# Kernel optimization log

Measured on AMD Instinct MI355X. Metric: run time of the kernel, lower is better.

## Reference

```python
import jax, jax.numpy as jnp
import numpy as np

N_NODES = 100000
N_EDGES = 3200000
IN_DIM = 4
BIG = 32
HID = 2
BN_EPS = 1e-5


def _lin_init(key, fan_in, fan_out):
    k1, k2 = jax.random.split(key)
    bound = 1.0 / np.sqrt(fan_in)
    W = jax.random.uniform(k1, (fan_in, fan_out), minval=-bound, maxval=bound, dtype=jnp.float32)
    b = jax.random.uniform(k2, (fan_out,), minval=-bound, maxval=bound, dtype=jnp.float32)
    return W, b


def setup_inputs() -> dict:
    key = jax.random.key(0)
    ks = jax.random.split(key, 12)
    x = jax.random.normal(ks[0], (N_NODES, IN_DIM), dtype=jnp.float32)
    edge_index = jax.random.randint(ks[1], (2, N_EDGES), 0, N_NODES, dtype=jnp.int32)
    eps_noise = jax.random.normal(ks[2], (N_NODES, HID), dtype=jnp.float32)
    # batchnorm affine params
    bn_gamma = jnp.ones((IN_DIM,), jnp.float32)
    bn_beta = jnp.zeros((IN_DIM,), jnp.float32)
    # encoder EdgeConv MLP: 2*IN_DIM -> BIG -> BIG
    eW1, eb1 = _lin_init(ks[3], 2 * IN_DIM, BIG)
    eW2, eb2 = _lin_init(ks[4], BIG, BIG)
    # mu / logvar heads
    mW, mb = _lin_init(ks[5], BIG, HID)
    vW, vb = _lin_init(ks[6], BIG, HID)
    # decoder EdgeConv MLP: 2*HID -> BIG -> BIG -> IN_DIM
    dW1, db1 = _lin_init(ks[7], 2 * HID, BIG)
    dW2, db2 = _lin_init(ks[8], BIG, BIG)
    dW3, db3 = _lin_init(ks[9], BIG, IN_DIM)
    return dict(x=x, edge_index=edge_index, eps_noise=eps_noise,
                bn_gamma=bn_gamma, bn_beta=bn_beta,
                eW1=eW1, eb1=eb1, eW2=eW2, eb2=eb2,
                mW=mW, mb=mb, vW=vW, vb=vb,
                dW1=dW1, db1=db1, dW2=dW2, db2=db2, dW3=dW3, db3=db3)


def _segment_mean(msgs, tgt, n):
    s = jax.ops.segment_sum(msgs, tgt, num_segments=n)
    c = jax.ops.segment_sum(jnp.ones((msgs.shape[0],), msgs.dtype), tgt, num_segments=n)
    return s / jnp.maximum(c, 1.0)[:, None]


def _edge_conv(x, edge_index, mlp):
    # PyG EdgeConv: h_i = mean_{j->i} nn([x_i, x_j - x_i])
    src, tgt = edge_index[0], edge_index[1]
    x_i = x[tgt]                      # [E, F]
    x_j = x[src]                      # [E, F]
    feat = jnp.concatenate([x_i, x_j - x_i], axis=-1)  # [E, 2F]
    msg = mlp(feat)                   # [E, F_out]
    return _segment_mean(msg, tgt, x.shape[0])


def reference(x, edge_index, eps_noise, bn_gamma, bn_beta,
              eW1, eb1, eW2, eb2, mW, mb, vW, vb,
              dW1, db1, dW2, db2, dW3, db3):
    # BatchNorm1d (training mode: batch statistics, biased variance)
    mean = jnp.mean(x, axis=0)
    var = jnp.var(x, axis=0)
    xn = (x - mean) * jax.lax.rsqrt(var + BN_EPS) * bn_gamma + bn_beta

    enc_mlp = lambda f: jax.nn.relu(jax.nn.relu(f @ eW1 + eb1) @ eW2 + eb2)
    h = _edge_conv(xn, edge_index, enc_mlp)           # [N, BIG]

    mu = h @ mW + mb                                  # [N, HID]
    log_var = h @ vW + vb                             # [N, HID]
    z = mu + eps_noise * jnp.exp(0.5 * log_var)       # reparameterize

    dec_mlp = lambda f: jax.nn.relu(jax.nn.relu(f @ dW1 + db1) @ dW2 + db2) @ dW3 + db3
    out = _edge_conv(z, edge_index, dec_mlp)          # [N, IN_DIM]
    return out, mu, log_var
```

## Files before the change

kernel.cpp:

```cpp
#include <hip/hip_runtime.h>
#include <math.h>

#define N_NODES 100000
#define N_EDGES 3200000
#define NBLK_EDGE ((N_EDGES + 255) / 256)
#define NBLK_NODE ((N_NODES + 255) / 256)

#define NB 64
#define NBUCK ((N_NODES + NB - 1) / NB)
#define NSLICE 256
#define SLICE (N_EDGES / NSLICE)
#define P2 2048

typedef _Float16 h2f16 __attribute__((ext_vector_type(2)));
typedef __fp16 f16x8 __attribute__((ext_vector_type(8)));
typedef float f32x4 __attribute__((ext_vector_type(4)));
typedef unsigned u32x4 __attribute__((ext_vector_type(4)));

#define PK_ENC_A2 0
#define PK_DEC_A2 512
#define PK_ENC_W1 1024
#define PK_DEC_W1 1152
#define PK_ENC_H 1216
#define PK_DEC_H 1280
#define PK_TOTAL 1344

__device__ __forceinline__ h2f16 mkh2(float a, float b) {
  h2f16 h;
  h.x = (_Float16)a;
  h.y = (_Float16)b;
  return h;
}
__device__ __forceinline__ float fdot2(h2f16 a, h2f16 b, float c) {
  return __builtin_amdgcn_fdot2(a, b, c, false);
}
__device__ __forceinline__ h2f16 pk(float a, float b) {
  auto r = __builtin_amdgcn_cvt_pkrtz(a, b);
  return __builtin_bit_cast(h2f16, r);
}
__device__ __forceinline__ unsigned h2u(h2f16 h) {
  return __builtin_bit_cast(unsigned, h);
}
__device__ __forceinline__ f32x4 mfma16(f16x8 a, f16x8 b, f32x4 c) {
  return __builtin_amdgcn_mfma_f32_16x16x32_f16(a, b, c, 0, 0, 0);
}

__global__ __launch_bounds__(256) void pack_weights(
    const float* __restrict__ eW1, const float* __restrict__ eW2,
    const float* __restrict__ mW, const float* __restrict__ vW,
    const float* __restrict__ dW1, const float* __restrict__ dW2,
    const float* __restrict__ dW3, h2f16* __restrict__ wpk) {
  int t = threadIdx.x;
  for (int i = t; i < 512; i += 256) {
    int tl = i >> 8, rest = i & 255, lane = rest >> 2, p = rest & 3;
    int q = lane >> 4, c = lane & 15;
    int k0 = q * 8 + 2 * p, out = 16 * tl + c;
    wpk[PK_ENC_A2 + i] = mkh2(eW2[k0 * 32 + out], eW2[(k0 + 1) * 32 + out]);
    wpk[PK_DEC_A2 + i] = mkh2(dW2[k0 * 32 + out], dW2[(k0 + 1) * 32 + out]);
  }
  for (int i = t; i < 128; i += 256) {
    int q = i >> 5, j = (i >> 2) & 7, kp = i & 3;
    wpk[PK_ENC_W1 + i] =
        mkh2(eW1[(2 * kp) * 32 + q * 8 + j], eW1[(2 * kp + 1) * 32 + q * 8 + j]);
  }
  for (int i = t; i < 64; i += 256) {
    int q = i >> 4, j = (i >> 1) & 7, kp = i & 1;
    wpk[PK_DEC_W1 + i] =
        mkh2(dW1[(2 * kp) * 32 + q * 8 + j], dW1[(2 * kp + 1) * 32 + q * 8 + j]);
  }
  for (int i = t; i < 64; i += 256) {
    int q = i >> 4, r = (i >> 2) & 3, h = i & 3;
    int o0 = 4 * q + r, o1 = 16 + 4 * q + r;
    float w0 = (h < 2) ? mW[o0 * 2 + h] : vW[o0 * 2 + (h - 2)];
    float w1 = (h < 2) ? mW[o1 * 2 + h] : vW[o1 * 2 + (h - 2)];
    wpk[PK_ENC_H + i] = mkh2(w0, w1);
    wpk[PK_DEC_H + i] = mkh2(dW3[o0 * 4 + h], dW3[o1 * 4 + h]);
  }
}

__global__ void bn_reduce(const float4* __restrict__ x, float* __restrict__ bns) {
  float s0 = 0, s1 = 0, s2 = 0, s3 = 0, q0 = 0, q1 = 0, q2 = 0, q3 = 0;
  for (int i = blockIdx.x * blockDim.x + threadIdx.x; i < N_NODES;
       i += gridDim.x * blockDim.x) {
    float4 v = x[i];
    s0 += v.x; s1 += v.y; s2 += v.z; s3 += v.w;
    q0 += v.x * v.x; q1 += v.y * v.y; q2 += v.z * v.z; q3 += v.w * v.w;
  }
#pragma unroll
  for (int o = 32; o; o >>= 1) {
    s0 += __shfl_down(s0, o); s1 += __shfl_down(s1, o);
    s2 += __shfl_down(s2, o); s3 += __shfl_down(s3, o);
    q0 += __shfl_down(q0, o); q1 += __shfl_down(q1, o);
    q2 += __shfl_down(q2, o); q3 += __shfl_down(q3, o);
  }
  __shared__ float red[4][8];
  int w = threadIdx.x >> 6;
  if ((threadIdx.x & 63) == 0) {
    red[w][0] = s0; red[w][1] = s1; red[w][2] = s2; red[w][3] = s3;
    red[w][4] = q0; red[w][5] = q1; red[w][6] = q2; red[w][7] = q3;
  }
  __syncthreads();
  if (threadIdx.x < 8) {
    float acc = red[0][threadIdx.x] + red[1][threadIdx.x] +
                red[2][threadIdx.x] + red[3][threadIdx.x];
    atomicAdd(&bns[threadIdx.x], acc);
  }
}

__global__ void bn_final(const float* __restrict__ bns,
                         const float* __restrict__ gamma,
                         const float* __restrict__ beta,
                         float* __restrict__ ab) {
  int d = threadIdx.x;
  if (d < 4) {
    float mean = bns[d] * (1.0f / N_NODES);
    float var = bns[4 + d] * (1.0f / N_NODES) - mean * mean;
    float a = gamma[d] * rsqrtf(var + 1e-5f);
    ab[d] = a;
    ab[4 + d] = beta[d] - mean * a;
  }
}

__global__ __launch_bounds__(256) void edge_hist(const int* __restrict__ tgt,
                                                 unsigned* __restrict__ hist) {
  __shared__ unsigned h[NBUCK];
  for (int i = threadIdx.x; i < NBUCK; i += 256) h[i] = 0;
  __syncthreads();
  int e0 = blockIdx.x * SLICE;
  for (int i = threadIdx.x; i < SLICE; i += 256)
    atomicAdd(&h[((unsigned)tgt[e0 + i]) >> 6], 1u);
  __syncthreads();
  for (int i = threadIdx.x; i < NBUCK; i += 256)
    hist[(size_t)blockIdx.x * NBUCK + i] = h[i];
}

__global__ __launch_bounds__(256) void bucket_tot(const unsigned* __restrict__ hist,
                                                  unsigned* __restrict__ tot) {
  int k = blockIdx.x * 256 + threadIdx.x;
  if (k >= NBUCK) return;
  unsigned s = 0;
#pragma unroll 8
  for (int b = 0; b < NSLICE; ++b) s += hist[(size_t)b * NBUCK + k];
  tot[k] = s;
}

__global__ __launch_bounds__(1024) void bucket_start(const unsigned* __restrict__ tot,
                                                     unsigned* __restrict__ start) {
  __shared__ unsigned sa[P2], sb[P2];
  for (int k = threadIdx.x; k < P2; k += 1024)
    sa[k] = (k < NBUCK) ? tot[k] : 0u;
  __syncthreads();
  unsigned *srcp = sa, *dstp = sb;
  for (int off = 1; off < P2; off <<= 1) {
    for (int k = threadIdx.x; k < P2; k += 1024)
      dstp[k] = srcp[k] + (k >= off ? srcp[k - off] : 0u);
    __syncthreads();
    unsigned* t = srcp; srcp = dstp; dstp = t;
  }
  for (int k = threadIdx.x; k <= NBUCK; k += 1024)
    start[k] = (k == 0) ? 0u : srcp[k - 1];
}

__global__ __launch_bounds__(256) void bucket_bases(unsigned* __restrict__ hist,
                                                    const unsigned* __restrict__ start) {
  int wv = threadIdx.x >> 6, lane = threadIdx.x & 63;
  int k = blockIdx.x * 4 + wv;
  if (k >= NBUCK) return;
  unsigned v0 = hist[(size_t)(4 * lane + 0) * NBUCK + k];
  unsigned v1 = hist[(size_t)(4 * lane + 1) * NBUCK + k];
  unsigned v2 = hist[(size_t)(4 * lane + 2) * NBUCK + k];
  unsigned v3 = hist[(size_t)(4 * lane + 3) * NBUCK + k];
  unsigned p1 = v0, p2 = v0 + v1, p3 = v0 + v1 + v2;
  unsigned s = p3 + v3;
  unsigned incl = s;
#pragma unroll
  for (int off = 1; off < 64; off <<= 1) {
    unsigned t = __shfl_up(incl, off);
    incl += (lane >= off) ? t : 0u;
  }
  unsigned base = start[k] + (incl - s);
  hist[(size_t)(4 * lane + 0) * NBUCK + k] = base;
  hist[(size_t)(4 * lane + 1) * NBUCK + k] = base + p1;
  hist[(size_t)(4 * lane + 2) * NBUCK + k] = base + p2;
  hist[(size_t)(4 * lane + 3) * NBUCK + k] = base + p3;
}

__global__ __launch_bounds__(256) void edge_place(
    const int* __restrict__ src, const int* __restrict__ tgt,
    const unsigned* __restrict__ hist, const unsigned* __restrict__ start,
    unsigned* __restrict__ payload) {
  __shared__ unsigned stage[SLICE];
  __shared__ unsigned offA[NBUCK];
  __shared__ unsigned A2[NBUCK];
  int s = blockIdx.x, tid = threadIdx.x;
  for (int k = tid; k < NBUCK; k += 256) {
    unsigned gb = hist[(size_t)s * NBUCK + k];
    unsigned nb = (s == NSLICE - 1) ? start[k + 1]
                                    : hist[(size_t)(s + 1) * NBUCK + k];
    offA[k] = gb;
    A2[k] = nb - gb;
  }
  __syncthreads();
  for (int d = 1; d < NBUCK; d <<= 1) {
    unsigned tmp[7];
    int m = 0;
    for (int k = tid; k < NBUCK; k += 256, ++m)
      tmp[m] = (k >= d) ? A2[k - d] : 0u;
    __syncthreads();
    m = 0;
    for (int k = tid; k < NBUCK; k += 256, ++m) A2[k] += tmp[m];
    __syncthreads();
  }
  {
    unsigned tmp[7];
    int m = 0;
    for (int k = tid; k < NBUCK; k += 256, ++m)
      tmp[m] = (k == 0) ? 0u : A2[k - 1];
    __syncthreads();
    m = 0;
    for (int k = tid; k < NBUCK; k += 256, ++m) {
      offA[k] -= tmp[m];
      A2[k] = tmp[m];
    }
    __syncthreads();
  }
  int e0 = s * SLICE;
  for (int i = tid; i < SLICE; i += 256) {
    unsigned t = (unsigned)tgt[e0 + i];
    unsigned sr = (unsigned)src[e0 + i];
    unsigned b = t >> 6;
    unsigned lp = atomicAdd(&A2[b], 1u);
    stage[lp] = sr | ((t & 63u) << 17);
  }
  __syncthreads();
  for (int b = tid; b < NBUCK; b += 256) {
    unsigned beg = (b == 0) ? 0u : A2[b - 1];
    unsigned end = A2[b];
    unsigned go = offA[b];
    for (unsigned i = beg; i < end; ++i) payload[go + i] = stage[i];
  }
}

__global__ __launch_bounds__(256) void enc_bucket(
    const float4* __restrict__ x, const unsigned* __restrict__ payload,
    const unsigned* __restrict__ start, const float* __restrict__ ab,
    const float* __restrict__ eb1, const float* __restrict__ eb2,
    const h2f16* __restrict__ wpk, float2* __restrict__ mpart,
    float2* __restrict__ vpart, float* __restrict__ cpart) {
  __shared__ float aM0[NB], aM1[NB], aV0[NB], aV1[NB], aC[NB];
  __shared__ float4 xt[NB];
  int k = blockIdx.x, node0 = k * NB, h = blockIdx.y;
  int tid = threadIdx.x, w = tid >> 6, lane = tid & 63;
  int q = lane >> 4, c = lane & 15;
  if (tid < NB) {
    int n = node0 + tid;
    aM0[tid] = 0; aM1[tid] = 0; aV0[tid] = 0; aV1[tid] = 0; aC[tid] = 0;
    xt[tid] = x[n < N_NODES ? n : 0];
  }
  __syncthreads();
  float a0 = ab[0], a1 = ab[1], a2 = ab[2], a3 = ab[3];
  float b0 = ab[4], b1 = ab[5], b2 = ab[6], b3 = ab[7];
  const u32x4* a2b = (const u32x4*)(wpk + PK_ENC_A2);
  f16x8 A0 = __builtin_bit_cast(f16x8, a2b[lane]);
  f16x8 A1 = __builtin_bit_cast(f16x8, a2b[64 + lane]);
  h2f16 w1e[32];
#pragma unroll
  for (int i = 0; i < 32; ++i) w1e[i] = wpk[PK_ENC_W1 + q * 32 + i];
  h2f16 hw[16];
#pragma unroll
  for (int i = 0; i < 16; ++i) hw[i] = wpk[PK_ENC_H + q * 16 + i];
  float eb1v[8];
#pragma unroll
  for (int j = 0; j < 8; ++j) eb1v[j] = eb1[q * 8 + j];
  float e2a[4], e2b[4];
#pragma unroll
  for (int r = 0; r < 4; ++r) {
    e2a[r] = eb2[4 * q + r];
    e2b[r] = eb2[16 + 4 * q + r];
  }
  unsigned s0v = start[k], s1v = start[k + 1];
  unsigned len = s1v - s0v, halfv = (len + 1) >> 1;
  unsigned lo = s0v + (h ? halfv : 0u);
  unsigned hi = h ? s1v : (s0v + halfv);
  for (unsigned base = lo + (unsigned)w * 32; base < hi; base += 128) {
    unsigned eA = base + (unsigned)c;
    unsigned eB = eA + 16;
    unsigned pA = payload[eA < hi ? eA : hi - 1];
    unsigned pB = payload[eB < hi ? eB : hi - 1];
    int siA = (int)(pA & 0x1FFFFu), siB = (int)(pB & 0x1FFFFu);
    int ltiA = (int)(pA >> 17), ltiB = (int)(pB >> 17);
    float4 xjA = x[siA];
    float4 xjB = x[siB];
    float4 xiA = xt[ltiA];
    float4 xiB = xt[ltiB];
    h2f16 fA0 = pk(fmaf(a0, xiA.x, b0), fmaf(a1, xiA.y, b1));
    h2f16 fA1 = pk(fmaf(a2, xiA.z, b2), fmaf(a3, xiA.w, b3));
    h2f16 fA2 = pk(a0 * (xjA.x - xiA.x), a1 * (xjA.y - xiA.y));
    h2f16 fA3 = pk(a2 * (xjA.z - xiA.z), a3 * (xjA.w - xiA.w));
    h2f16 fB0 = pk(fmaf(a0, xiB.x, b0), fmaf(a1, xiB.y, b1));
    h2f16 fB1 = pk(fmaf(a2, xiB.z, b2), fmaf(a3, xiB.w, b3));
    h2f16 fB2 = pk(a0 * (xjB.x - xiB.x), a1 * (xjB.y - xiB.y));
    h2f16 fB3 = pk(a2 * (xjB.z - xiB.z), a3 * (xjB.w - xiB.w));
    float rA[8], rB[8];
#pragma unroll
    for (int j = 0; j < 8; ++j) {
      float uA = eb1v[j], uB = eb1v[j];
      uA = fdot2(fA0, w1e[4 * j + 0], uA);
      uB = fdot2(fB0, w1e[4 * j + 0], uB);
      uA = fdot2(fA1, w1e[4 * j + 1], uA);
      uB = fdot2(fB1, w1e[4 * j + 1], uB);
      uA = fdot2(fA2, w1e[4 * j + 2], uA);
      uB = fdot2(fB2, w1e[4 * j + 2], uB);
      uA = fdot2(fA3, w1e[4 * j + 3], uA);
      uB = fdot2(fB3, w1e[4 * j + 3], uB);
      rA[j] = fmaxf(uA, 0.0f);
      rB[j] = fmaxf(uB, 0.0f);
    }
    u32x4 buA, buB;
    buA[0] = h2u(pk(rA[0], rA[1])); buA[1] = h2u(pk(rA[2], rA[3]));
    buA[2] = h2u(pk(rA[4], rA[5])); buA[3] = h2u(pk(rA[6], rA[7]));
    buB[0] = h2u(pk(rB[0], rB[1])); buB[1] = h2u(pk(rB[2], rB[3]));
    buB[2] = h2u(pk(rB[4], rB[5])); buB[3] = h2u(pk(rB[6], rB[7]));
    f16x8 BA = __builtin_bit_cast(f16x8, buA);
    f16x8 BB = __builtin_bit_cast(f16x8, buB);
    f32x4 zf = {0.f, 0.f, 0.f, 0.f};
    f32x4 C0A = mfma16(A0, BA, zf), C1A = mfma16(A1, BA, zf);
    f32x4 C0B = mfma16(A0, BB, zf), C1B = mfma16(A1, BB, zf);
    float m0A = 0, m1A = 0, v0A = 0, v1A = 0;
    float m0B = 0, m1B = 0, v0B = 0, v1B = 0;
#pragma unroll
    for (int rr = 0; rr < 4; ++rr) {
      h2f16 hA = pk(fmaxf(C0A[rr] + e2a[rr], 0.0f),
                    fmaxf(C1A[rr] + e2b[rr], 0.0f));
      h2f16 hB = pk(fmaxf(C0B[rr] + e2a[rr], 0.0f),
                    fmaxf(C1B[rr] + e2b[rr], 0.0f));
      m0A = fdot2(hA, hw[4 * rr + 0], m0A);
      m0B = fdot2(hB, hw[4 * rr + 0], m0B);
      m1A = fdot2(hA, hw[4 * rr + 1], m1A);
      m1B = fdot2(hB, hw[4 * rr + 1], m1B);
      v0A = fdot2(hA, hw[4 * rr + 2], v0A);
      v0B = fdot2(hB, hw[4 * rr + 2], v0B);
      v1A = fdot2(hA, hw[4 * rr + 3], v1A);
      v1B = fdot2(hB, hw[4 * rr + 3], v1B);
    }
    m0A += __shfl_xor(m0A, 16); m0A += __shfl_xor(m0A, 32);
    m1A += __shfl_xor(m1A, 16); m1A += __shfl_xor(m1A, 32);
    v0A += __shfl_xor(v0A, 16); v0A += __shfl_xor(v0A, 32);
    v1A += __shfl_xor(v1A, 16); v1A += __shfl_xor(v1A, 32);
    m0B += __shfl_xor(m0B, 16); m0B += __shfl_xor(m0B, 32);
    m1B += __shfl_xor(m1B, 16); m1B += __shfl_xor(m1B, 32);
    v0B += __shfl_xor(v0B, 16); v0B += __shfl_xor(v0B, 32);
    v1B += __shfl_xor(v1B, 16); v1B += __shfl_xor(v1B, 32);
    if (lane < 16) {
      if (eA < hi) {
        atomicAdd(&aM0[ltiA], m0A);
        atomicAdd(&aM1[ltiA], m1A);
        atomicAdd(&aV0[ltiA], v0A);
        atomicAdd(&aV1[ltiA], v1A);
        atomicAdd(&aC[ltiA], 1.0f);
      }
      if (eB < hi) {
        atomicAdd(&aM0[ltiB], m0B);
        atomicAdd(&aM1[ltiB], m1B);
        atomicAdd(&aV0[ltiB], v0B);
        atomicAdd(&aV1[ltiB], v1B);
        atomicAdd(&aC[ltiB], 1.0f);
      }
    }
  }
  __syncthreads();
  if (tid < NB) {
    int n = node0 + tid;
    if (n < N_NODES) {
      mpart[(size_t)h * N_NODES + n] = make_float2(aM0[tid], aM1[tid]);
      vpart[(size_t)h * N_NODES + n] = make_float2(aV0[tid], aV1[tid]);
      cpart[(size_t)h * N_NODES + n] = aC[tid];
    }
  }
}

__global__ __launch_bounds__(256) void node_mid(
    const float2* __restrict__ mpart, const float2* __restrict__ vpart,
    const float* __restrict__ cpart, const float* __restrict__ eps2,
    const float* __restrict__ mbias, const float* __restrict__ vbias,
    float* __restrict__ z, float* __restrict__ cntC,
    float2* __restrict__ muOut, float2* __restrict__ lvOut) {
  int n = blockIdx.x * 256 + threadIdx.x;
  if (n >= N_NODES) return;
  float2 ma = mpart[n], mb2 = mpart[N_NODES + n];
  float2 va = vpart[n], vb2 = vpart[N_NODES + n];
  float cc = cpart[n] + cpart[N_NODES + n];
  float inv = 1.0f / fmaxf(cc, 1.0f);
  float mu0 = fmaf(ma.x + mb2.x, inv, mbias[0]);
  float mu1 = fmaf(ma.y + mb2.y, inv, mbias[1]);
  float lv0 = fmaf(va.x + vb2.x, inv, vbias[0]);
  float lv1 = fmaf(va.y + vb2.y, inv, vbias[1]);
  cntC[n] = cc;
  muOut[n] = make_float2(mu0, mu1);
  lvOut[n] = make_float2(lv0, lv1);
  z[2 * n + 0] = fmaf(eps2[2 * n + 0], expf(0.5f * lv0), mu0);
  z[2 * n + 1] = fmaf(eps2[2 * n + 1], expf(0.5f * lv1), mu1);
}

__global__ __launch_bounds__(256) void dec_bucket(
    const float2* __restrict__ z, const unsigned* __restrict__ payload,
    const unsigned* __restrict__ start, const float* __restrict__ db1,
    const float* __restrict__ db2, const float* __restrict__ db3,
    const h2f16* __restrict__ wpk, float4* __restrict__ opart) {
  __shared__ float aO0[NB], aO1[NB], aO2[NB], aO3[NB];
  __shared__ float2 zt[NB];
  int k = blockIdx.x, node0 = k * NB, h = blockIdx.y;
  int tid = threadIdx.x, w = tid >> 6, lane = tid & 63;
  int q = lane >> 4, c = lane & 15;
  if (tid < NB) {
    int n = node0 + tid;
    aO0[tid] = 0; aO1[tid] = 0; aO2[tid] = 0; aO3[tid] = 0;
    zt[tid] = z[n < N_NODES ? n : 0];
  }
  __syncthreads();
  const u32x4* a2b = (const u32x4*)(wpk + PK_DEC_A2);
  f16x8 A0 = __builtin_bit_cast(f16x8, a2b[lane]);
  f16x8 A1 = __builtin_bit_cast(f16x8, a2b[64 + lane]);
  h2f16 w1d[16];
#pragma unroll
  for (int i = 0; i < 16; ++i) w1d[i] = wpk[PK_DEC_W1 + q * 16 + i];
  h2f16 hw[16];
#pragma unroll
  for (int i = 0; i < 16; ++i) hw[i] = wpk[PK_DEC_H + q * 16 + i];
  float db1v[8];
#pragma unroll
  for (int j = 0; j < 8; ++j) db1v[j] = db1[q * 8 + j];
  float d2a[4], d2b[4];
#pragma unroll
  for (int r = 0; r < 4; ++r) {
    d2a[r] = db2[4 * q + r];
    d2b[r] = db2[16 + 4 * q + r];
  }
  float b3_0 = db3[0], b3_1 = db3[1], b3_2 = db3[2], b3_3 = db3[3];
  unsigned s0v = start[k], s1v = start[k + 1];
  unsigned len = s1v - s0v, halfv = (len + 1) >> 1;
  unsigned lo = s0v + (h ? halfv : 0u);
  unsigned hi = h ? s1v : (s0v + halfv);
  for (unsigned base = lo + (unsigned)w * 32; base < hi; base += 128) {
    unsigned eA = base + (unsigned)c;
    unsigned eB = eA + 16;
    unsigned pA = payload[eA < hi ? eA : hi - 1];
    unsigned pB = payload[eB < hi ? eB : hi - 1];
    int siA = (int)(pA & 0x1FFFFu), siB = (int)(pB & 0x1FFFFu);
    int ltiA = (int)(pA >> 17), ltiB = (int)(pB >> 17);
    float2 zjA = z[siA];
    float2 zjB = z[siB];
    float2 ziA = zt[ltiA];
    float2 ziB = zt[ltiB];
    h2f16 fA0 = pk(ziA.x, ziA.y);
    h2f16 fA1 = pk(zjA.x - ziA.x, zjA.y - ziA.y);
    h2f16 fB0 = pk(ziB.x, ziB.y);
    h2f16 fB1 = pk(zjB.x - ziB.x, zjB.y - ziB.y);
    float rA[8], rB[8];
#pragma unroll
    for (int j = 0; j < 8; ++j) {
      float uA = db1v[j], uB = db1v[j];
      uA = fdot2(fA0, w1d[2 * j + 0], uA);
      uB = fdot2(fB0, w1d[2 * j + 0], uB);
      uA = fdot2(fA1, w1d[2 * j + 1], uA);
      uB = fdot2(fB1, w1d[2 * j + 1], uB);
      rA[j] = fmaxf(uA, 0.0f);
      rB[j] = fmaxf(uB, 0.0f);
    }
    u32x4 buA, buB;
    buA[0] = h2u(pk(rA[0], rA[1])); buA[1] = h2u(pk(rA[2], rA[3]));
    buA[2] = h2u(pk(rA[4], rA[5])); buA[3] = h2u(pk(rA[6], rA[7]));
    buB[0] = h2u(pk(rB[0], rB[1])); buB[1] = h2u(pk(rB[2], rB[3]));
    buB[2] = h2u(pk(rB[4], rB[5])); buB[3] = h2u(pk(rB[6], rB[7]));
    f16x8 BA = __builtin_bit_cast(f16x8, buA);
    f16x8 BB = __builtin_bit_cast(f16x8, buB);
    f32x4 zf = {0.f, 0.f, 0.f, 0.f};
    f32x4 C0A = mfma16(A0, BA, zf), C1A = mfma16(A1, BA, zf);
    f32x4 C0B = mfma16(A0, BB, zf), C1B = mfma16(A1, BB, zf);
    float o0A = 0, o1A = 0, o2A = 0, o3A = 0;
    float o0B = 0, o1B = 0, o2B = 0, o3B = 0;
#pragma unroll
    for (int rr = 0; rr < 4; ++rr) {
      h2f16 hA = pk(fmaxf(C0A[rr] + d2a[rr], 0.0f),
                    fmaxf(C1A[rr] + d2b[rr], 0.0f));
      h2f16 hB = pk(fmaxf(C0B[rr] + d2a[rr], 0.0f),
                    fmaxf(C1B[rr] + d2b[rr], 0.0f));
      o0A = fdot2(hA, hw[4 * rr + 0], o0A);
      o0B = fdot2(hB, hw[4 * rr + 0], o0B);
      o1A = fdot2(hA, hw[4 * rr + 1], o1A);
      o1B = fdot2(hB, hw[4 * rr + 1], o1B);
      o2A = fdot2(hA, hw[4 * rr + 2], o2A);
      o2B = fdot2(hB, hw[4 * rr + 2], o2B);
      o3A = fdot2(hA, hw[4 * rr + 3], o3A);
      o3B = fdot2(hB, hw[4 * rr + 3], o3B);
    }
    o0A += __shfl_xor(o0A, 16); o0A += __shfl_xor(o0A, 32);
    o1A += __shfl_xor(o1A, 16); o1A += __shfl_xor(o1A, 32);
    o2A += __shfl_xor(o2A, 16); o2A += __shfl_xor(o2A, 32);
    o3A += __shfl_xor(o3A, 16); o3A += __shfl_xor(o3A, 32);
    o0B += __shfl_xor(o0B, 16); o0B += __shfl_xor(o0B, 32);
    o1B += __shfl_xor(o1B, 16); o1B += __shfl_xor(o1B, 32);
    o2B += __shfl_xor(o2B, 16); o2B += __shfl_xor(o2B, 32);
    o3B += __shfl_xor(o3B, 16); o3B += __shfl_xor(o3B, 32);
    if (lane < 16) {
      if (eA < hi) {
        atomicAdd(&aO0[ltiA], o0A + b3_0);
        atomicAdd(&aO1[ltiA], o1A + b3_1);
        atomicAdd(&aO2[ltiA], o2A + b3_2);
        atomicAdd(&aO3[ltiA], o3A + b3_3);
      }
      if (eB < hi) {
        atomicAdd(&aO0[ltiB], o0B + b3_0);
        atomicAdd(&aO1[ltiB], o1B + b3_1);
        atomicAdd(&aO2[ltiB], o2B + b3_2);
        atomicAdd(&aO3[ltiB], o3B + b3_3);
      }
    }
  }
  __syncthreads();
  if (tid < NB) {
    int n = node0 + tid;
    if (n < N_NODES)
      opart[(size_t)h * N_NODES + n] =
          make_float4(aO0[tid], aO1[tid], aO2[tid], aO3[tid]);
  }
}

__global__ __launch_bounds__(256) void node_final(
    const float4* __restrict__ opart, const float* __restrict__ cntC,
    float4* __restrict__ outp) {
  int n = blockIdx.x * 256 + threadIdx.x;
  if (n >= N_NODES) return;
  float4 a = opart[n], b = opart[N_NODES + n];
  float inv = 1.0f / fmaxf(cntC[n], 1.0f);
  outp[n] = make_float4((a.x + b.x) * inv, (a.y + b.y) * inv,
                        (a.z + b.z) * inv, (a.w + b.w) * inv);
}

__device__ __forceinline__ void atomAddF(float* p, float v) {
  unsafeAtomicAdd(p, v);
}

__global__ __launch_bounds__(256) void enc_edge_fb(
    const float4* __restrict__ x, const int* __restrict__ esrc,
    const int* __restrict__ etgt, const float* __restrict__ ab,
    const float* __restrict__ eW1, const float* __restrict__ eb1,
    const float* __restrict__ eW2, const float* __restrict__ eb2,
    const float* __restrict__ mW, const float* __restrict__ vW,
    float* __restrict__ msum, float* __restrict__ vsum,
    float* __restrict__ cnt) {
  int e = blockIdx.x * 256 + threadIdx.x;
  if (e >= N_EDGES) return;
  int si = esrc[e], ti = etgt[e];
  float4 xi = x[ti];
  float4 xj = x[si];
  float a0 = ab[0], a1 = ab[1], a2 = ab[2], a3 = ab[3];
  float b0 = ab[4], b1 = ab[5], b2 = ab[6], b3 = ab[7];
  float feat[8];
  feat[0] = fmaf(a0, xi.x, b0);
  feat[1] = fmaf(a1, xi.y, b1);
  feat[2] = fmaf(a2, xi.z, b2);
  feat[3] = fmaf(a3, xi.w, b3);
  feat[4] = a0 * (xj.x - xi.x);
  feat[5] = a1 * (xj.y - xi.y);
  feat[6] = a2 * (xj.z - xi.z);
  feat[7] = a3 * (xj.w - xi.w);
  float h1[32];
#pragma unroll 8
  for (int j = 0; j < 32; ++j) {
    float acc = eb1[j];
#pragma unroll
    for (int kk = 0; kk < 8; ++kk) acc = fmaf(feat[kk], eW1[kk * 32 + j], acc);
    h1[j] = fmaxf(acc, 0.0f);
  }
  float m0 = 0, m1 = 0, v0 = 0, v1 = 0;
#pragma unroll 4
  for (int j = 0; j < 32; ++j) {
    float acc = eb2[j];
#pragma unroll
    for (int kk = 0; kk < 32; ++kk) acc = fmaf(h1[kk], eW2[kk * 32 + j], acc);
    float h2 = fmaxf(acc, 0.0f);
    m0 = fmaf(h2, mW[j * 2 + 0], m0);
    m1 = fmaf(h2, mW[j * 2 + 1], m1);
    v0 = fmaf(h2, vW[j * 2 + 0], v0);
    v1 = fmaf(h2, vW[j * 2 + 1], v1);
  }
  atomAddF(&msum[ti * 2 + 0], m0);
  atomAddF(&msum[ti * 2 + 1], m1);
  atomAddF(&vsum[ti * 2 + 0], v0);
  atomAddF(&vsum[ti * 2 + 1], v1);
  atomAddF(&cnt[ti], 1.0f);
}

__global__ __launch_bounds__(256) void dec_edge_fb(
    const float2* __restrict__ z, const int* __restrict__ esrc,
    const int* __restrict__ etgt, const float* __restrict__ dW1,
    const float* __restrict__ db1, const float* __restrict__ dW2,
    const float* __restrict__ db2, const float* __restrict__ dW3,
    const float* __restrict__ db3, float* __restrict__ osum) {
  int e = blockIdx.x * 256 + threadIdx.x;
  if (e >= N_EDGES) return;
  int si = esrc[e], ti = etgt[e];
  float2 zi = z[ti], zj = z[si];
  float f0 = zi.x, f1 = zi.y, f2 = zj.x - zi.x, f3 = zj.y - zi.y;
  float h1[32];
#pragma unroll 8
  for (int j = 0; j < 32; ++j) {
    float acc = db1[j];
    acc = fmaf(f0, dW1[0 * 32 + j], acc);
    acc = fmaf(f1, dW1[1 * 32 + j], acc);
    acc = fmaf(f2, dW1[2 * 32 + j], acc);
    acc = fmaf(f3, dW1[3 * 32 + j], acc);
    h1[j] = fmaxf(acc, 0.0f);
  }
  float o0 = db3[0], o1 = db3[1], o2 = db3[2], o3 = db3[3];
#pragma unroll 4
  for (int j = 0; j < 32; ++j) {
    float acc = db2[j];
#pragma unroll
    for (int kk = 0; kk < 32; ++kk) acc = fmaf(h1[kk], dW2[kk * 32 + j], acc);
    float h2 = fmaxf(acc, 0.0f);
    o0 = fmaf(h2, dW3[j * 4 + 0], o0);
    o1 = fmaf(h2, dW3[j * 4 + 1], o1);
    o2 = fmaf(h2, dW3[j * 4 + 2], o2);
    o3 = fmaf(h2, dW3[j * 4 + 3], o3);
  }
  atomAddF(&osum[4 * ti + 0], o0);
  atomAddF(&osum[4 * ti + 1], o1);
  atomAddF(&osum[4 * ti + 2], o2);
  atomAddF(&osum[4 * ti + 3], o3);
}

__global__ __launch_bounds__(256) void node_mid_fb(
    float* __restrict__ msum, float* __restrict__ vsum,
    const float* __restrict__ cnt, const float* __restrict__ eps2,
    const float* __restrict__ mb, const float* __restrict__ vb,
    float* __restrict__ z) {
  int n = blockIdx.x * 256 + threadIdx.x;
  if (n >= N_NODES) return;
  float inv = 1.0f / fmaxf(cnt[n], 1.0f);
  float mu0 = fmaf(msum[2 * n + 0], inv, mb[0]);
  float mu1 = fmaf(msum[2 * n + 1], inv, mb[1]);
  float lv0 = fmaf(vsum[2 * n + 0], inv, vb[0]);
  float lv1 = fmaf(vsum[2 * n + 1], inv, vb[1]);
  msum[2 * n + 0] = mu0;
  msum[2 * n + 1] = mu1;
  vsum[2 * n + 0] = lv0;
  vsum[2 * n + 1] = lv1;
  z[2 * n + 0] = fmaf(eps2[2 * n + 0], expf(0.5f * lv0), mu0);
  z[2 * n + 1] = fmaf(eps2[2 * n + 1], expf(0.5f * lv1), mu1);
}

__global__ __launch_bounds__(256) void node_final_fb(
    float* __restrict__ osum, const float* __restrict__ cnt) {
  int n = blockIdx.x * 256 + threadIdx.x;
  if (n >= N_NODES) return;
  float inv = 1.0f / fmaxf(cnt[n], 1.0f);
  float4* o4 = (float4*)osum;
  float4 v = o4[n];
  v.x *= inv; v.y *= inv; v.z *= inv; v.w *= inv;
  o4[n] = v;
}

extern "C" void kernel_launch(void* const* d_in, const int* in_sizes, int n_in,
                              void* d_out, int out_size, void* d_ws,
                              size_t ws_size, hipStream_t stream) {
  const float* x = (const float*)d_in[0];
  const int* ei = (const int*)d_in[1];
  const float* eps = (const float*)d_in[2];
// ... 79 lines not shown
```

Before: 403.4 us.

## Move first-layer and head matmuls onto MFMA and software-pipeline edge gathers

Result: faster. 368.9 us (-8.5%).

```diff
diff --git a/kernel.cpp b/kernel.cpp
--- a/kernel.cpp
+++ b/kernel.cpp
@@ -19,11 +19,11 @@
 
 #define PK_ENC_A2 0
 #define PK_DEC_A2 512
-#define PK_ENC_W1 1024
-#define PK_DEC_W1 1152
-#define PK_ENC_H 1216
-#define PK_DEC_H 1280
-#define PK_TOTAL 1344
+#define PK_ENC_A1 1024
+#define PK_DEC_A1 1536
+#define PK_ENC_HA 2048
+#define PK_DEC_HA 2304
+#define PK_TOTAL 2560
 
 __device__ __forceinline__ h2f16 mkh2(float a, float b) {
   h2f16 h;
@@ -54,27 +54,37 @@
   for (int i = t; i < 512; i += 256) {
     int tl = i >> 8, rest = i & 255, lane = rest >> 2, p = rest & 3;
     int q = lane >> 4, c = lane & 15;
-    int k0 = q * 8 + 2 * p, out = 16 * tl + c;
+    int out = 16 * tl + c;
+    int k0 = (p < 2) ? (4 * q + 2 * p) : (16 + 4 * q + 2 * (p - 2));
     wpk[PK_ENC_A2 + i] = mkh2(eW2[k0 * 32 + out], eW2[(k0 + 1) * 32 + out]);
     wpk[PK_DEC_A2 + i] = mkh2(dW2[k0 * 32 + out], dW2[(k0 + 1) * 32 + out]);
   }
-  for (int i = t; i < 128; i += 256) {
-    int q = i >> 5, j = (i >> 2) & 7, kp = i & 3;
-    wpk[PK_ENC_W1 + i] =
-        mkh2(eW1[(2 * kp) * 32 + q * 8 + j], eW1[(2 * kp + 1) * 32 + q * 8 + j]);
-  }
-  for (int i = t; i < 64; i += 256) {
-    int q = i >> 4, j = (i >> 1) & 7, kp = i & 1;
-    wpk[PK_DEC_W1 + i] =
-        mkh2(dW1[(2 * kp) * 32 + q * 8 + j], dW1[(2 * kp + 1) * 32 + q * 8 + j]);
-  }
-  for (int i = t; i < 64; i += 256) {
-    int q = i >> 4, r = (i >> 2) & 3, h = i & 3;
-    int o0 = 4 * q + r, o1 = 16 + 4 * q + r;
-    float w0 = (h < 2) ? mW[o0 * 2 + h] : vW[o0 * 2 + (h - 2)];
-    float w1 = (h < 2) ? mW[o1 * 2 + h] : vW[o1 * 2 + (h - 2)];
-    wpk[PK_ENC_H + i] = mkh2(w0, w1);
-    wpk[PK_DEC_H + i] = mkh2(dW3[o0 * 4 + h], dW3[o1 * 4 + h]);
+  for (int i = t; i < 512; i += 256) {
+    int tl = i >> 8, rest = i & 255, lane = rest >> 2, p = rest & 3;
+    int q = lane >> 4, c = lane & 15;
+    int out = 16 * tl + c;
+    int k0 = 8 * q + 2 * p;
+    float w0e = (k0 < 8) ? eW1[k0 * 32 + out] : 0.0f;
+    float w1e = (k0 + 1 < 8) ? eW1[(k0 + 1) * 32 + out] : 0.0f;
+    float w0d = (k0 < 4) ? dW1[k0 * 32 + out] : 0.0f;
+    float w1d = (k0 + 1 < 4) ? dW1[(k0 + 1) * 32 + out] : 0.0f;
+    wpk[PK_ENC_A1 + i] = mkh2(w0e, w1e);
+    wpk[PK_DEC_A1 + i] = mkh2(w0d, w1d);
+  }
+  for (int i = t; i < 256; i += 256) {
+    int lane = i >> 2, p = i & 3;
+    int q = lane >> 4, c = lane & 15;
+    int d0 = (p < 2) ? (4 * q + 2 * p) : (16 + 4 * q + 2 * (p - 2));
+    int d1 = d0 + 1;
+    float e0 = 0.f, e1 = 0.f, g0 = 0.f, g1 = 0.f;
+    if (c < 4) {
+      e0 = (c < 2) ? mW[d0 * 2 + c] : vW[d0 * 2 + (c - 2)];
+      e1 = (c < 2) ? mW[d1 * 2 + c] : vW[d1 * 2 + (c - 2)];
+      g0 = dW3[d0 * 4 + c];
+      g1 = dW3[d1 * 4 + c];
+    }
+    wpk[PK_ENC_HA + i] = mkh2(e0, e1);
+    wpk[PK_DEC_HA + i] = mkh2(g0, g1);
   }
 }
 
@@ -241,7 +251,7 @@
   }
 }
 
-__global__ __launch_bounds__(256) void enc_bucket(
+__global__ __launch_bounds__(256, 4) void enc_bucket(
     const float4* __restrict__ x, const unsigned* __restrict__ payload,
     const unsigned* __restrict__ start, const float* __restrict__ ab,
     const float* __restrict__ eb1, const float* __restrict__ eb2,
@@ -260,21 +270,19 @@
   __syncthreads();
   float a0 = ab[0], a1 = ab[1], a2 = ab[2], a3 = ab[3];
   float b0 = ab[4], b1 = ab[5], b2 = ab[6], b3 = ab[7];
-  const u32x4* a2b = (const u32x4*)(wpk + PK_ENC_A2);
-  f16x8 A0 = __builtin_bit_cast(f16x8, a2b[lane]);
-  f16x8 A1 = __builtin_bit_cast(f16x8, a2b[64 + lane]);
-  h2f16 w1e[32];
-#pragma unroll
-  for (int i = 0; i < 32; ++i) w1e[i] = wpk[PK_ENC_W1 + q * 32 + i];
-  h2f16 hw[16];
-#pragma unroll
-  for (int i = 0; i < 16; ++i) hw[i] = wpk[PK_ENC_H + q * 16 + i];
-  float eb1v[8];
-#pragma unroll
-  for (int j = 0; j < 8; ++j) eb1v[j] = eb1[q * 8 + j];
-  float e2a[4], e2b[4];
+  const u32x4* a2t = (const u32x4*)(wpk + PK_ENC_A2);
+  const u32x4* a1t = (const u32x4*)(wpk + PK_ENC_A1);
+  const u32x4* hat = (const u32x4*)(wpk + PK_ENC_HA);
+  f16x8 A20 = __builtin_bit_cast(f16x8, a2t[lane]);
+  f16x8 A21 = __builtin_bit_cast(f16x8, a2t[64 + lane]);
+  f16x8 A10 = __builtin_bit_cast(f16x8, a1t[lane]);
+  f16x8 A11 = __builtin_bit_cast(f16x8, a1t[64 + lane]);
+  f16x8 HA = __builtin_bit_cast(f16x8, hat[lane]);
+  float e1a[4], e1b[4], e2a[4], e2b[4];
 #pragma unroll
   for (int r = 0; r < 4; ++r) {
+    e1a[r] = eb1[4 * q + r];
+    e1b[r] = eb1[16 + 4 * q + r];
     e2a[r] = eb2[4 * q + r];
     e2b[r] = eb2[16 + 4 * q + r];
   }
@@ -282,90 +290,84 @@
   unsigned len = s1v - s0v, halfv = (len + 1) >> 1;
   unsigned lo = s0v + (h ? halfv : 0u);
   unsigned hi = h ? s1v : (s0v + halfv);
-  for (unsigned base = lo + (unsigned)w * 32; base < hi; base += 128) {
+  unsigned base = lo + (unsigned)w * 32u;
+  if (base < hi) {
     unsigned eA = base + (unsigned)c;
-    unsigned eB = eA + 16;
-    unsigned pA = payload[eA < hi ? eA : hi - 1];
-    unsigned pB = payload[eB < hi ? eB : hi - 1];
-    int siA = (int)(pA & 0x1FFFFu), siB = (int)(pB & 0x1FFFFu);
-    int ltiA = (int)(pA >> 17), ltiB = (int)(pB >> 17);
-    float4 xjA = x[siA];
-    float4 xjB = x[siB];
-    float4 xiA = xt[ltiA];
-    float4 xiB = xt[ltiB];
-    h2f16 fA0 = pk(fmaf(a0, xiA.x, b0), fmaf(a1, xiA.y, b1));
-    h2f16 fA1 = pk(fmaf(a2, xiA.z, b2), fmaf(a3, xiA.w, b3));
-    h2f16 fA2 = pk(a0 * (xjA.x - xiA.x), a1 * (xjA.y - xiA.y));
-    h2f16 fA3 = pk(a2 * (xjA.z - xiA.z), a3 * (xjA.w - xiA.w));
-    h2f16 fB0 = pk(fmaf(a0, xiB.x, b0), fmaf(a1, xiB.y, b1));
-    h2f16 fB1 = pk(fmaf(a2, xiB.z, b2), fmaf(a3, xiB.w, b3));
-    h2f16 fB2 = pk(a0 * (xjB.x - xiB.x), a1 * (xjB.y - xiB.y));
-    h2f16 fB3 = pk(a2 * (xjB.z - xiB.z), a3 * (xjB.w - xiB.w));
-    float rA[8], rB[8];
-#pragma unroll
-    for (int j = 0; j < 8; ++j) {
-      float uA = eb1v[j], uB = eb1v[j];
-      uA = fdot2(fA0, w1e[4 * j + 0], uA);
-      uB = fdot2(fB0, w1e[4 * j + 0], uB);
-      uA = fdot2(fA1, w1e[4 * j + 1], uA);
-      uB = fdot2(fB1, w1e[4 * j + 1], uB);
-      uA = fdot2(fA2, w1e[4 * j + 2], uA);
-      uB = fdot2(fB2, w1e[4 * j + 2], uB);
-      uA = fdot2(fA3, w1e[4 * j + 3], uA);
-      uB = fdot2(fB3, w1e[4 * j + 3], uB);
-      rA[j] = fmaxf(uA, 0.0f);
-      rB[j] = fmaxf(uB, 0.0f);
-    }
-    u32x4 buA, buB;
-    buA[0] = h2u(pk(rA[0], rA[1])); buA[1] = h2u(pk(rA[2], rA[3]));
-    buA[2] = h2u(pk(rA[4], rA[5])); buA[3] = h2u(pk(rA[6], rA[7]));
-    buB[0] = h2u(pk(rB[0], rB[1])); buB[1] = h2u(pk(rB[2], rB[3]));
-    buB[2] = h2u(pk(rB[4], rB[5])); buB[3] = h2u(pk(rB[6], rB[7]));
-    f16x8 BA = __builtin_bit_cast(f16x8, buA);
-    f16x8 BB = __builtin_bit_cast(f16x8, buB);
+    eA = eA < hi ? eA : hi - 1u;
+    unsigned eB = base + 16u + (unsigned)c;
+    eB = eB < hi ? eB : hi - 1u;
+    unsigned pA = payload[eA], pB = payload[eB];
+    float4 xjA = x[(int)(pA & 0x1FFFFu)];
+    float4 xjB = x[(int)(pB & 0x1FFFFu)];
     f32x4 zf = {0.f, 0.f, 0.f, 0.f};
-    f32x4 C0A = mfma16(A0, BA, zf), C1A = mfma16(A1, BA, zf);
-    f32x4 C0B = mfma16(A0, BB, zf), C1B = mfma16(A1, BB, zf);
-    float m0A = 0, m1A = 0, v0A = 0, v1A = 0;
-    float m0B = 0, m1B = 0, v0B = 0, v1B = 0;
-#pragma unroll
-    for (int rr = 0; rr < 4; ++rr) {
-      h2f16 hA = pk(fmaxf(C0A[rr] + e2a[rr], 0.0f),
-                    fmaxf(C1A[rr] + e2b[rr], 0.0f));
-      h2f16 hB = pk(fmaxf(C0B[rr] + e2a[rr], 0.0f),
-                    fmaxf(C1B[rr] + e2b[rr], 0.0f));
-      m0A = fdot2(hA, hw[4 * rr + 0], m0A);
-      m0B = fdot2(hB, hw[4 * rr + 0], m0B);
-      m1A = fdot2(hA, hw[4 * rr + 1], m1A);
-      m1B = fdot2(hB, hw[4 * rr + 1], m1B);
-      v0A = fdot2(hA, hw[4 * rr + 2], v0A);
-      v0B = fdot2(hB, hw[4 * rr + 2], v0B);
-      v1A = fdot2(hA, hw[4 * rr + 3], v1A);
-      v1B = fdot2(hB, hw[4 * rr + 3], v1B);
-    }
-    m0A += __shfl_xor(m0A, 16); m0A += __shfl_xor(m0A, 32);
-    m1A += __shfl_xor(m1A, 16); m1A += __shfl_xor(m1A, 32);
-    v0A += __shfl_xor(v0A, 16); v0A += __shfl_xor(v0A, 32);
-    v1A += __shfl_xor(v1A, 16); v1A += __shfl_xor(v1A, 32);
-    m0B += __shfl_xor(m0B, 16); m0B += __shfl_xor(m0B, 32);
-    m1B += __shfl_xor(m1B, 16); m1B += __shfl_xor(m1B, 32);
-    v0B += __shfl_xor(v0B, 16); v0B += __shfl_xor(v0B, 32);
-    v1B += __shfl_xor(v1B, 16); v1B += __shfl_xor(v1B, 32);
-    if (lane < 16) {
-      if (eA < hi) {
-        atomicAdd(&aM0[ltiA], m0A);
-        atomicAdd(&aM1[ltiA], m1A);
-        atomicAdd(&aV0[ltiA], v0A);
-        atomicAdd(&aV1[ltiA], v1A);
-        atomicAdd(&aC[ltiA], 1.0f);
+    for (; base < hi; base += 128u) {
+      unsigned nb = base + 128u;
+      unsigned eAn = nb + (unsigned)c;
+      eAn = eAn < hi ? eAn : hi - 1u;
+      unsigned eBn = nb + 16u + (unsigned)c;
+      eBn = eBn < hi ? eBn : hi - 1u;
+      unsigned pAn = payload[eAn];
+      unsigned pBn = payload[eBn];
+      int ltiA = (int)(pA >> 17), ltiB = (int)(pB >> 17);
+      float4 xiA = xt[ltiA], xiB = xt[ltiB];
+      bool vA = (base + (unsigned)c) < hi;
+      bool vB = (base + 16u + (unsigned)c) < hi;
+      u32x4 fuA, fuB;
+      fuA[0] = h2u(pk(fmaf(a0, xiA.x, b0), fmaf(a1, xiA.y, b1)));
+      fuA[1] = h2u(pk(fmaf(a2, xiA.z, b2), fmaf(a3, xiA.w, b3)));
+      fuA[2] = h2u(pk(a0 * (xjA.x - xiA.x), a1 * (xjA.y - xiA.y)));
+      fuA[3] = h2u(pk(a2 * (xjA.z - xiA.z), a3 * (xjA.w - xiA.w)));
+      fuB[0] = h2u(pk(fmaf(a0, xiB.x, b0), fmaf(a1, xiB.y, b1)));
+      fuB[1] = h2u(pk(fmaf(a2, xiB.z, b2), fmaf(a3, xiB.w, b3)));
+      fuB[2] = h2u(pk(a0 * (xjB.x - xiB.x), a1 * (xjB.y - xiB.y)));
+      fuB[3] = h2u(pk(a2 * (xjB.z - xiB.z), a3 * (xjB.w - xiB.w)));
+      float4 xjAn = x[(int)(pAn & 0x1FFFFu)];
+      float4 xjBn = x[(int)(pBn & 0x1FFFFu)];
+      f16x8 FA = __builtin_bit_cast(f16x8, fuA);
+      f16x8 FB = __builtin_bit_cast(f16x8, fuB);
+      f32x4 D10A = mfma16(A10, FA, zf), D11A = mfma16(A11, FA, zf);
+      f32x4 D10B = mfma16(A10, FB, zf), D11B = mfma16(A11, FB, zf);
+      u32x4 h1A, h1B;
+      h1A[0] = h2u(pk(fmaxf(D10A[0] + e1a[0], 0.f), fmaxf(D10A[1] + e1a[1], 0.f)));
+      h1A[1] = h2u(pk(fmaxf(D10A[2] + e1a[2], 0.f), fmaxf(D10A[3] + e1a[3], 0.f)));
+      h1A[2] = h2u(pk(fmaxf(D11A[0] + e1b[0], 0.f), fmaxf(D11A[1] + e1b[1], 0.f)));
+      h1A[3] = h2u(pk(fmaxf(D11A[2] + e1b[2], 0.f), fmaxf(D11A[3] + e1b[3], 0.f)));
+      h1B[0] = h2u(pk(fmaxf(D10B[0] + e1a[0], 0.f), fmaxf(D10B[1] + e1a[1], 0.f)));
+      h1B[1] = h2u(pk(fmaxf(D10B[2] + e1a[2], 0.f), fmaxf(D10B[3] + e1a[3], 0.f)));
+      h1B[2] = h2u(pk(fmaxf(D11B[0] + e1b[0], 0.f), fmaxf(D11B[1] + e1b[1], 0.f)));
+      h1B[3] = h2u(pk(fmaxf(D11B[2] + e1b[2], 0.f), fmaxf(D11B[3] + e1b[3], 0.f)));
+      f16x8 B2A = __builtin_bit_cast(f16x8, h1A);
+      f16x8 B2B = __builtin_bit_cast(f16x8, h1B);
+      f32x4 C0A = mfma16(A20, B2A, zf), C1A = mfma16(A21, B2A, zf);
+      f32x4 C0B = mfma16(A20, B2B, zf), C1B = mfma16(A21, B2B, zf);
+      u32x4 g2A, g2B;
+      g2A[0] = h2u(pk(fmaxf(C0A[0] + e2a[0], 0.f), fmaxf(C0A[1] + e2a[1], 0.f)));
+      g2A[1] = h2u(pk(fmaxf(C0A[2] + e2a[2], 0.f), fmaxf(C0A[3] + e2a[3], 0.f)));
+      g2A[2] = h2u(pk(fmaxf(C1A[0] + e2b[0], 0.f), fmaxf(C1A[1] + e2b[1], 0.f)));
+      g2A[3] = h2u(pk(fmaxf(C1A[2] + e2b[2], 0.f), fmaxf(C1A[3] + e2b[3], 0.f)));
+      g2B[0] = h2u(pk(fmaxf(C0B[0] + e2a[0], 0.f), fmaxf(C0B[1] + e2a[1], 0.f)));
+      g2B[1] = h2u(pk(fmaxf(C0B[2] + e2a[2], 0.f), fmaxf(C0B[3] + e2a[3], 0.f)));
+      g2B[2] = h2u(pk(fmaxf(C1B[0] + e2b[0], 0.f), fmaxf(C1B[1] + e2b[1], 0.f)));
+      g2B[3] = h2u(pk(fmaxf(C1B[2] + e2b[2], 0.f), fmaxf(C1B[3] + e2b[3], 0.f)));
+      f32x4 D2A = mfma16(HA, __builtin_bit_cast(f16x8, g2A), zf);
+      f32x4 D2B = mfma16(HA, __builtin_bit_cast(f16x8, g2B), zf);
+      if (lane < 16) {
+        if (vA) {
+          atomicAdd(&aM0[ltiA], D2A[0]);
+          atomicAdd(&aM1[ltiA], D2A[1]);
+          atomicAdd(&aV0[ltiA], D2A[2]);
+          atomicAdd(&aV1[ltiA], D2A[3]);
+          atomicAdd(&aC[ltiA], 1.0f);
+        }
+        if (vB) {
+          atomicAdd(&aM0[ltiB], D2B[0]);
+          atomicAdd(&aM1[ltiB], D2B[1]);
+          atomicAdd(&aV0[ltiB], D2B[2]);
+          atomicAdd(&aV1[ltiB], D2B[3]);
+          atomicAdd(&aC[ltiB], 1.0f);
+        }
       }
-      if (eB < hi) {
-        atomicAdd(&aM0[ltiB], m0B);
-        atomicAdd(&aM1[ltiB], m1B);
-        atomicAdd(&aV0[ltiB], v0B);
-        atomicAdd(&aV1[ltiB], v1B);
-        atomicAdd(&aC[ltiB], 1.0f);
-      }
+      pA = pAn; pB = pBn; xjA = xjAn; xjB = xjBn;
     }
   }
   __syncthreads();
@@ -402,7 +404,7 @@
   z[2 * n + 1] = fmaf(eps2[2 * n + 1], expf(0.5f * lv1), mu1);
 }
 
-__global__ __launch_bounds__(256) void dec_bucket(
+__global__ __launch_bounds__(256, 4) void dec_bucket(
     const float2* __restrict__ z, const unsigned* __restrict__ payload,
     const unsigned* __restrict__ start, const float* __restrict__ db1,
     const float* __restrict__ db2, const float* __restrict__ db3,
@@ -418,103 +420,103 @@
     zt[tid] = z[n < N_NODES ? n : 0];
   }
   __syncthreads();
-  const u32x4* a2b = (const u32x4*)(wpk + PK_DEC_A2);
-  f16x8 A0 = __builtin_bit_cast(f16x8, a2b[lane]);
-  f16x8 A1 = __builtin_bit_cast(f16x8, a2b[64 + lane]);
-  h2f16 w1d[16];
-#pragma unroll
-  for (int i = 0; i < 16; ++i) w1d[i] = wpk[PK_DEC_W1 + q * 16 + i];
-  h2f16 hw[16];
-#pragma unroll
-  for (int i = 0; i < 16; ++i) hw[i] = wpk[PK_DEC_H + q * 16 + i];
-  float db1v[8];
-#pragma unroll
-  for (int j = 0; j < 8; ++j) db1v[j] = db1[q * 8 + j];
-  float d2a[4], d2b[4];
+  const u32x4* a2t = (const u32x4*)(wpk + PK_DEC_A2);
+  const u32x4* a1t = (const u32x4*)(wpk + PK_DEC_A1);
+  const u32x4* hat = (const u32x4*)(wpk + PK_DEC_HA);
+  f16x8 A20 = __builtin_bit_cast(f16x8, a2t[lane]);
+  f16x8 A21 = __builtin_bit_cast(f16x8, a2t[64 + lane]);
+  f16x8 A10 = __builtin_bit_cast(f16x8, a1t[lane]);
+  f16x8 A11 = __builtin_bit_cast(f16x8, a1t[64 + lane]);
+  f16x8 HA = __builtin_bit_cast(f16x8, hat[lane]);
+  float e1a[4], e1b[4], e2a[4], e2b[4];
 #pragma unroll
   for (int r = 0; r < 4; ++r) {
-    d2a[r] = db2[4 * q + r];
-    d2b[r] = db2[16 + 4 * q + r];
+    e1a[r] = db1[4 * q + r];
+    e1b[r] = db1[16 + 4 * q + r];
+    e2a[r] = db2[4 * q + r];
+    e2b[r] = db2[16 + 4 * q + r];
   }
   float b3_0 = db3[0], b3_1 = db3[1], b3_2 = db3[2], b3_3 = db3[3];
   unsigned s0v = start[k], s1v = start[k + 1];
   unsigned len = s1v - s0v, halfv = (len + 1) >> 1;
   unsigned lo = s0v + (h ? halfv : 0u);
   unsigned hi = h ? s1v : (s0v + halfv);
-  for (unsigned base = lo + (unsigned)w * 32; base < hi; base += 128) {
+  unsigned base = lo + (unsigned)w * 32u;
+  if (base < hi) {
     unsigned eA = base + (unsigned)c;
-    unsigned eB = eA + 16;
-    unsigned pA = payload[eA < hi ? eA : hi - 1];
-    unsigned pB = payload[eB < hi ? eB : hi - 1];
-    int siA = (int)(pA & 0x1FFFFu), siB = (int)(pB & 0x1FFFFu);
-    int ltiA = (int)(pA >> 17), ltiB = (int)(pB >> 17);
-    float2 zjA = z[siA];
-    float2 zjB = z[siB];
-    float2 ziA = zt[ltiA];
-    float2 ziB = zt[ltiB];
-    h2f16 fA0 = pk(ziA.x, ziA.y);
-    h2f16 fA1 = pk(zjA.x - ziA.x, zjA.y - ziA.y);
-    h2f16 fB0 = pk(ziB.x, ziB.y);
-    h2f16 fB1 = pk(zjB.x - ziB.x, zjB.y - ziB.y);
-    float rA[8], rB[8];
-#pragma unroll
-    for (int j = 0; j < 8; ++j) {
-      float uA = db1v[j], uB = db1v[j];
-      uA = fdot2(fA0, w1d[2 * j + 0], uA);
-      uB = fdot2(fB0, w1d[2 * j + 0], uB);
-      uA = fdot2(fA1, w1d[2 * j + 1], uA);
-      uB = fdot2(fB1, w1d[2 * j + 1], uB);
-      rA[j] = fmaxf(uA, 0.0f);
-      rB[j] = fmaxf(uB, 0.0f);
-    }
-    u32x4 buA, buB;
-    buA[0] = h2u(pk(rA[0], rA[1])); buA[1] = h2u(pk(rA[2], rA[3]));
-    buA[2] = h2u(pk(rA[4], rA[5])); buA[3] = h2u(pk(rA[6], rA[7]));
-    buB[0] = h2u(pk(rB[0], rB[1])); buB[1] = h2u(pk(rB[2], rB[3]));
-    buB[2] = h2u(pk(rB[4], rB[5])); buB[3] = h2u(pk(rB[6], rB[7]));
-    f16x8 BA = __builtin_bit_cast(f16x8, buA);
-    f16x8 BB = __builtin_bit_cast(f16x8, buB);
+    eA = eA < hi ? eA : hi - 1u;
+    unsigned eB = base + 16u + (unsigned)c;
+    eB = eB < hi ? eB : hi - 1u;
+    unsigned pA = payload[eA], pB = payload[eB];
+    float2 zjA = z[(int)(pA & 0x1FFFFu)];
+    float2 zjB = z[(int)(pB & 0x1FFFFu)];
     f32x4 zf = {0.f, 0.f, 0.f, 0.f};
-    f32x4 C0A = mfma16(A0, BA, zf), C1A = mfma16(A1, BA, zf);
-    f32x4 C0B = mfma16(A0, BB, zf), C1B = mfma16(A1, BB, zf);
-    float o0A = 0, o1A = 0, o2A = 0, o3A = 0;
-    float o0B = 0, o1B = 0, o2B = 0, o3B = 0;
-#pragma unroll
-    for (int rr = 0; rr < 4; ++rr) {
-      h2f16 hA = pk(fmaxf(C0A[rr] + d2a[rr], 0.0f),
-                    fmaxf(C1A[rr] + d2b[rr], 0.0f));
-      h2f16 hB = pk(fmaxf(C0B[rr] + d2a[rr], 0.0f),
-                    fmaxf(C1B[rr] + d2b[rr], 0.0f));
-      o0A = fdot2(hA, hw[4 * rr + 0], o0A);
-      o0B = fdot2(hB, hw[4 * rr + 0], o0B);
-      o1A = fdot2(hA, hw[4 * rr + 1], o1A);
-      o1B = fdot2(hB, hw[4 * rr + 1], o1B);
-      o2A = fdot2(hA, hw[4 * rr + 2], o2A);
-      o2B = fdot2(hB, hw[4 * rr + 2], o2B);
-      o3A = fdot2(hA, hw[4 * rr + 3], o3A);
-      o3B = fdot2(hB, hw[4 * rr + 3], o3B);
-    }
-    o0A += __shfl_xor(o0A, 16); o0A += __shfl_xor(o0A, 32);
-    o1A += __shfl_xor(o1A, 16); o1A += __shfl_xor(o1A, 32);
-    o2A += __shfl_xor(o2A, 16); o2A += __shfl_xor(o2A, 32);
-    o3A += __shfl_xor(o3A, 16); o3A += __shfl_xor(o3A, 32);
-    o0B += __shfl_xor(o0B, 16); o0B += __shfl_xor(o0B, 32);
-    o1B += __shfl_xor(o1B, 16); o1B += __shfl_xor(o1B, 32);
-    o2B += __shfl_xor(o2B, 16); o2B += __shfl_xor(o2B, 32);
-    o3B += __shfl_xor(o3B, 16); o3B += __shfl_xor(o3B, 32);
-    if (lane < 16) {
-      if (eA < hi) {
-        atomicAdd(&aO0[ltiA], o0A + b3_0);
-        atomicAdd(&aO1[ltiA], o1A + b3_1);
-        atomicAdd(&aO2[ltiA], o2A + b3_2);
-        atomicAdd(&aO3[ltiA], o3A + b3_3);
+    for (; base < hi; base += 128u) {
+      unsigned nb = base + 128u;
+      unsigned eAn = nb + (unsigned)c;
+      eAn = eAn < hi ? eAn : hi - 1u;
+      unsigned eBn = nb + 16u + (unsigned)c;
+      eBn = eBn < hi ? eBn : hi - 1u;
+      unsigned pAn = payload[eAn];
+      unsigned pBn = payload[eBn];
+      int ltiA = (int)(pA >> 17), ltiB = (int)(pB >> 17);
+      float2 ziA = zt[ltiA], ziB = zt[ltiB];
+      bool vA = (base + (unsigned)c) < hi;
+      bool vB = (base + 16u + (unsigned)c) < hi;
+      u32x4 fuA, fuB;
+      fuA[0] = h2u(pk(ziA.x, ziA.y));
+      fuA[1] = h2u(pk(zjA.x - ziA.x, zjA.y - ziA.y));
+      fuA[2] = fuA[0];
+      fuA[3] = fuA[1];
+      fuB[0] = h2u(pk(ziB.x, ziB.y));
+      fuB[1] = h2u(pk(zjB.x - ziB.x, zjB.y - ziB.y));
+      fuB[2] = fuB[0];
+      fuB[3] = fuB[1];
+      float2 zjAn = z[(int)(pAn & 0x1FFFFu)];
+      float2 zjBn = z[(int)(pBn & 0x1FFFFu)];
+      f16x8 FA = __builtin_bit_cast(f16x8, fuA);
+      f16x8 FB = __builtin_bit_cast(f16x8, fuB);
+      f32x4 D10A = mfma16(A10, FA, zf), D11A = mfma16(A11, FA, zf);
+      f32x4 D10B = mfma16(A10, FB, zf), D11B = mfma16(A11, FB, zf);
+      u32x4 h1A, h1B;
+      h1A[0] = h2u(pk(fmaxf(D10A[0] + e1a[0], 0.f), fmaxf(D10A[1] + e1a[1], 0.f)));
+      h1A[1] = h2u(pk(fmaxf(D10A[2] + e1a[2], 0.f), fmaxf(D10A[3] + e1a[3], 0.f)));
+      h1A[2] = h2u(pk(fmaxf(D11A[0] + e1b[0], 0.f), fmaxf(D11A[1] + e1b[1], 0.f)));
+      h1A[3] = h2u(pk(fmaxf(D11A[2] + e1b[2], 0.f), fmaxf(D11A[3] + e1b[3], 0.f)));
+      h1B[0] = h2u(pk(fmaxf(D10B[0] + e1a[0], 0.f), fmaxf(D10B[1] + e1a[1], 0.f)));
+      h1B[1] = h2u(pk(fmaxf(D10B[2] + e1a[2], 0.f), fmaxf(D10B[3] + e1a[3], 0.f)));
+      h1B[2] = h2u(pk(fmaxf(D11B[0] + e1b[0], 0.f), fmaxf(D11B[1] + e1b[1], 0.f)));
+      h1B[3] = h2u(pk(fmaxf(D11B[2] + e1b[2], 0.f), fmaxf(D11B[3] + e1b[3], 0.f)));
+      f16x8 B2A = __builtin_bit_cast(f16x8, h1A);
+      f16x8 B2B = __builtin_bit_cast(f16x8, h1B);
+      f32x4 C0A = mfma16(A20, B2A, zf), C1A = mfma16(A21, B2A, zf);
+      f32x4 C0B = mfma16(A20, B2B, zf), C1B = mfma16(A21, B2B, zf);
+      u32x4 g2A, g2B;
+      g2A[0] = h2u(pk(fmaxf(C0A[0] + e2a[0], 0.f), fmaxf(C0A[1] + e2a[1], 0.f)));
+      g2A[1] = h2u(pk(fmaxf(C0A[2] + e2a[2], 0.f), fmaxf(C0A[3] + e2a[3], 0.f)));
+      g2A[2] = h2u(pk(fmaxf(C1A[0] + e2b[0], 0.f), fmaxf(C1A[1] + e2b[1], 0.f)));
+      g2A[3] = h2u(pk(fmaxf(C1A[2] + e2b[2], 0.f), fmaxf(C1A[3] + e2b[3], 0.f)));
+      g2B[0] = h2u(pk(fmaxf(C0B[0] + e2a[0], 0.f), fmaxf(C0B[1] + e2a[1], 0.f)));
+      g2B[1] = h2u(pk(fmaxf(C0B[2] + e2a[2], 0.f), fmaxf(C0B[3] + e2a[3], 0.f)));
+      g2B[2] = h2u(pk(fmaxf(C1B[0] + e2b[0], 0.f), fmaxf(C1B[1] + e2b[1], 0.f)));
+      g2B[3] = h2u(pk(fmaxf(C1B[2] + e2b[2], 0.f), fmaxf(C1B[3] + e2b[3], 0.f)));
+      f32x4 D2A = mfma16(HA, __builtin_bit_cast(f16x8, g2A), zf);
+      f32x4 D2B = mfma16(HA, __builtin_bit_cast(f16x8, g2B), zf);
+      if (lane < 16) {
+        if (vA) {
+          atomicAdd(&aO0[ltiA], D2A[0] + b3_0);
+          atomicAdd(&aO1[ltiA], D2A[1] + b3_1);
+          atomicAdd(&aO2[ltiA], D2A[2] + b3_2);
+          atomicAdd(&aO3[ltiA], D2A[3] + b3_3);
+        }
+        if (vB) {
+          atomicAdd(&aO0[ltiB], D2B[0] + b3_0);
+          atomicAdd(&aO1[ltiB], D2B[1] + b3_1);
+          atomicAdd(&aO2[ltiB], D2B[2] + b3_2);
+          atomicAdd(&aO3[ltiB], D2B[3] + b3_3);
+        }
       }
-      if (eB < hi) {
-        atomicAdd(&aO0[ltiB], o0B + b3_0);
-        atomicAdd(&aO1[ltiB], o1B + b3_1);
-        atomicAdd(&aO2[ltiB], o2B + b3_2);
-        atomicAdd(&aO3[ltiB], o3B + b3_3);
-      }
+      pA = pAn; pB = pBn; zjA = zjAn; zjB = zjBn;
     }
   }
   __syncthreads();
```
